# Performance work log

Hardware: AMD Instinct MI355X
Metric: run time of the kernel (lower is better)

## Reference

```python
import jax, jax.numpy as jnp
import numpy as np

N = 1_000_000
HID = 128
S = 10_000

def setup_inputs() -> dict:
    key = jax.random.key(0)
    k1, k2, k3, k4, k5 = jax.random.split(key, 5)
    seg_embs = jax.random.normal(k1, (N, HID), dtype=jnp.float32)
    owners = jnp.sort(jax.random.randint(k2, (N,), 0, S, dtype=jnp.int64))
    W_proj = jax.random.normal(k3, (HID, HID), dtype=jnp.float32) * (1.0 / np.sqrt(HID))
    b_proj = jax.random.normal(k4, (HID,), dtype=jnp.float32) * 0.02
    w_score = jax.random.normal(k5, (HID,), dtype=jnp.float32) * (1.0 / np.sqrt(HID))
    b_score = jnp.zeros((), dtype=jnp.float32)
    return {"seg_embs": seg_embs, "owners": owners, "W_proj": W_proj,
            "b_proj": b_proj, "w_score": w_score, "b_score": b_score,
            "num_segments": S}

def reference(seg_embs, owners, W_proj, b_proj, w_score, b_score, num_segments):
    # H = tanh(Linear(seg_embs)); u = score(H)  -> [N]
    H = jnp.tanh(seg_embs @ W_proj.T + b_proj)            # [N, hid]
    u = H @ w_score + b_score                              # [N]
    # per-owner (segment) stable softmax
    umax = jax.ops.segment_max(u, owners, num_segments=num_segments)   # [S]
    e = jnp.exp(u - umax[owners])                          # [N]
    denom = jax.ops.segment_sum(e, owners, num_segments=num_segments)  # [S]
    a = e / denom[owners]                                  # [N]
    # weighted sum of seg_embs per owner -> [S, hid]
    z = jax.ops.segment_sum(a[:, None] * seg_embs, owners, num_segments=num_segments)
    return z
```

## Files before the change

### kernel.cpp

```cpp
#include <hip/hip_runtime.h>
#include <hip/hip_bf16.h>
#include <cmath>

#define HID 128
#define TM 64
#define MAXK 8
#define PIECE_F 132
#define XP 132

typedef __attribute__((ext_vector_type(8))) short bf16x8;
typedef __attribute__((ext_vector_type(16))) float f32x16;
typedef __attribute__((ext_vector_type(4))) float f32x4;
typedef __attribute__((ext_vector_type(2))) float f32x2;

__device__ __forceinline__ float exp2_fast(float x) {
    float r;
    asm("v_exp_f32 %0, %1" : "=v"(r) : "v"(x));
    return r;
}

__device__ __forceinline__ bf16x8 pack8(const float* f) {
    union { short h8[8]; bf16x8 v; } u;
    #pragma unroll
    for (int q = 0; q < 8; ++q)
        u.h8[q] = (short)__bfloat16_as_ushort(__float2bfloat16(f[q]));
    return u.v;
}

__device__ __forceinline__ void tanh4(const float* arg, const float* w, float& s) {
    float a0 = exp2_fast(arg[0]) + 1.0f;
    float a1 = exp2_fast(arg[1]) + 1.0f;
    float a2 = exp2_fast(arg[2]) + 1.0f;
    float a3 = exp2_fast(arg[3]) + 1.0f;
    float p01 = a0 * a1, p23 = a2 * a3;
    float r = __builtin_amdgcn_rcpf(p01 * p23);
    float r01 = r * p23, r23 = r * p01;
    float i0 = r01 * a1, i1 = r01 * a0;
    float i2 = r23 * a3, i3 = r23 * a2;
    s = fmaf(w[0], fmaf(-2.0f, i0, 1.0f), s);
    s = fmaf(w[1], fmaf(-2.0f, i1, 1.0f), s);
    s = fmaf(w[2], fmaf(-2.0f, i2, 1.0f), s);
    s = fmaf(w[3], fmaf(-2.0f, i3, 1.0f), s);
}

__global__ __launch_bounds__(256) void prep_w_frag(
    const float* __restrict__ W, short* __restrict__ whi)
{
    int id = blockIdx.x * 256 + threadIdx.x;
    int l  = id & 63;
    int kc = (id >> 6) & 7;
    int wv = id >> 9;
    int j  = wv * 32 + (l & 31);
    int k0 = kc * 16 + ((l >> 5) << 3);
    const float* src = W + j * HID + k0;
    float a8[8];
    #pragma unroll
    for (int q = 0; q < 8; ++q) a8[q] = src[q];
    *(bf16x8*)(whi + (size_t)id * 8) = pack8(a8);
}

__global__ void seg_start_kernel(const int* __restrict__ ow,
                                 int* __restrict__ seg_start,
                                 int* __restrict__ fseg, int N, int S)
{
    const int is64 = (ow[(size_t)N - 1] == 0) ? 1 : 0;
    long i = (long)blockIdx.x * blockDim.x + threadIdx.x;
    if (i > N) return;
    int a = (i == 0) ? -1 : ow[is64 ? (size_t)(2 * (i - 1)) : (size_t)(i - 1)];
    int b = (i == N) ? S  : ow[is64 ? (size_t)(2 * i)       : (size_t)i];
    for (int s = a + 1; s <= b; ++s) seg_start[s] = (int)i;
    if (i < N && (i & (TM - 1)) == 0) fseg[i >> 6] = b;
}

__global__ __launch_bounds__(256, 6) void fused_kernel(
    const float* __restrict__ X, const short* __restrict__ whi_g,
    const float* __restrict__ bproj, const float* __restrict__ wscore,
    const int* __restrict__ seg_start, const int* __restrict__ fseg,
    float* __restrict__ pieces, int N, int S)
{
    __shared__ __align__(16) short X_lds[TM * XP];
    __shared__ float u_part[4][TM];
    __shared__ float w_lds[TM];
    __shared__ float bw_lds[2 * HID];

    const int tid  = threadIdx.x;
    const int bIdx = blockIdx.x;
    const int rbase = bIdx * TM;
    const int limit = (N - rbase < TM) ? (N - rbase) : TM;

    const int lane = tid & 63;
    const int wv   = tid >> 6;
    const int l31  = lane & 31;
    const int hig  = lane >> 5;

    const int sseg0 = fseg[bIdx];
    int svl = sseg0 + lane;
    int sv  = seg_start[(svl <= S) ? svl : S];

    #pragma unroll
    for (int it = 0; it < 4; ++it) {
        int id = it * 256 + tid;
        int r  = id >> 4;
        int c  = id & 15;
        int grow = rbase + r;
        if (grow >= N) grow = N - 1;
        float a8[8];
        *(f32x4*)(a8)     = *(const f32x4*)(X + (size_t)grow * HID + c * 8);
        *(f32x4*)(a8 + 4) = *(const f32x4*)(X + (size_t)grow * HID + c * 8 + 4);
        *(bf16x8*)(&X_lds[r * XP + c * 8]) = pack8(a8);
    }
    if (tid < HID) {
        bw_lds[2 * tid]     = 2.885390082f * bproj[tid];
        bw_lds[2 * tid + 1] = wscore[tid];
    }
    __syncthreads();

    f32x16 acc0, acc1;
    #pragma unroll
    for (int g = 0; g < 16; ++g) { acc0[g] = 0.0f; acc1[g] = 0.0f; }

    const short* wbase = whi_g + (size_t)(wv * 8) * 64 * 8 + (size_t)lane * 8;
    #pragma unroll
    for (int kc = 0; kc < 8; ++kc) {
        bf16x8 wfk = *(const bf16x8*)(wbase + (size_t)kc * 64 * 8);
        int c = kc * 2 + hig;
        bf16x8 x0 = *(const bf16x8*)(&X_lds[l31 * XP + c * 8]);
        bf16x8 x1 = *(const bf16x8*)(&X_lds[(32 + l31) * XP + c * 8]);
        acc0 = __builtin_amdgcn_mfma_f32_32x32x16_bf16(wfk, x0, acc0, 0, 0, 0);
        acc1 = __builtin_amdgcn_mfma_f32_32x32x16_bf16(wfk, x1, acc1, 0, 0, 0);
    }

    float s0 = 0.0f, s1 = 0.0f;
    #pragma unroll
    for (int g4 = 0; g4 < 4; ++g4) {
        float arg0[4], arg1[4], w4[4];
        #pragma unroll
        for (int q = 0; q < 4; ++q) {
            int reg = g4 * 4 + q;
            int j = wv * 32 + (reg & 3) + ((reg >> 2) << 3) + (hig << 2);
            f32x2 bw = *(const f32x2*)(&bw_lds[2 * j]);
            arg0[q] = fmaf(2.885390082f, acc0[reg], bw.x);
            arg1[q] = fmaf(2.885390082f, acc1[reg], bw.x);
            w4[q]   = bw.y;
        }
        tanh4(arg0, w4, s0);
        tanh4(arg1, w4, s1);
    }
    s0 += __shfl_xor(s0, 32, 64);
    s1 += __shfl_xor(s1, 32, 64);
    if (hig == 0) {
        u_part[wv][l31]      = s0;
        u_part[wv][32 + l31] = s1;
    }
    __syncthreads();

    for (int i = wv; ; i += 4) {
        int st, en;
        if (i < 63) {
            st = __shfl(sv, i, 64);
            en = __shfl(sv, i + 1, 64);
        } else {
            int s0i = sseg0 + i;
            st = seg_start[(s0i     <= S) ? s0i     : S];
            en = seg_start[(s0i + 1 <= S) ? s0i + 1 : S];
        }
        if (st >= rbase + limit) break;
        if (en <= st) continue;
        int a  = st - rbase; if (a < 0) a = 0;
        int bb = en - rbase; if (bb > limit) bb = limit;
        if (a >= bb) continue;

        float uv = -INFINITY;
        if (a + lane < bb)
            uv = u_part[0][a + lane] + u_part[1][a + lane]
               + u_part[2][a + lane] + u_part[3][a + lane];
        float m = uv;
        #pragma unroll
        for (int o = 32; o > 0; o >>= 1) m = fmaxf(m, __shfl_xor(m, o, 64));
        float e0 = (a + lane < bb) ? exp2_fast((uv - m) * 1.442695041f) : 0.0f;
        float d = e0;
        #pragma unroll
        for (int o = 32; o > 0; o >>= 1) d += __shfl_xor(d, o, 64);
        if (a + lane < bb) w_lds[a + lane] = e0;

        f32x2 p = {0.0f, 0.0f};
        int rr = a;
        for (; rr + 4 <= bb; rr += 4) {
            #pragma unroll
            for (int q = 0; q < 4; ++q) {
                int rc = rr + q;
                float wq = w_lds[rc];
                unsigned pr = *(const unsigned*)(&X_lds[rc * XP + 2 * lane]);
                float x0 = __builtin_bit_cast(float, pr << 16);
                float x1 = __builtin_bit_cast(float, pr & 0xFFFF0000u);
                p.x = fmaf(wq, x0, p.x);
                p.y = fmaf(wq, x1, p.y);
            }
        }
        for (; rr < bb; ++rr) {
            float wq = w_lds[rr];
            unsigned pr = *(const unsigned*)(&X_lds[rr * XP + 2 * lane]);
            float x0 = __builtin_bit_cast(float, pr << 16);
            float x1 = __builtin_bit_cast(float, pr & 0xFFFF0000u);
            p.x = fmaf(wq, x0, p.x);
            p.y = fmaf(wq, x1, p.y);
        }

        int sseg = sseg0 + i;
        int slot = (bIdx - (st >> 6)) & (MAXK - 1);
        float* dst = pieces + ((size_t)sseg * MAXK + slot) * PIECE_F;
        if (lane == 0) { dst[0] = m; dst[1] = d; }
        *(f32x2*)(dst + 4 + 2 * lane) = p;
    }
}

__global__ __launch_bounds__(64) void fixup_kernel(
    const float* __restrict__ pieces, const int* __restrict__ seg_start,
    float* __restrict__ z)
{
    const int s = blockIdx.x;
    const int lane = threadIdx.x;
    const int start = seg_start[s];
    const int end   = seg_start[s + 1];

    if (start >= end) {
        f32x2 zo = {0.0f, 0.0f};
        *(f32x2*)(z + (size_t)s * HID + lane * 2) = zo;
        return;
    }
    int K = ((end - 1) >> 6) - (start >> 6) + 1;
    if (K > MAXK) K = MAXK;

    const float* base0 = pieces + (size_t)s * MAXK * PIECE_F;
    float M = -INFINITY;
    for (int k = 0; k < K; ++k) M = fmaxf(M, base0[k * PIECE_F]);

    float D = 0.0f;
    f32x2 zz = {0.0f, 0.0f};
    for (int k = 0; k < K; ++k) {
        const float* b = base0 + k * PIECE_F;
        float sc = __expf(b[0] - M);
        D = fmaf(b[1], sc, D);
        f32x2 pv = *(const f32x2*)(b + 4 + lane * 2);
        zz.x = fmaf(sc, pv.x, zz.x);
        zz.y = fmaf(sc, pv.y, zz.y);
    }
    float inv = 1.0f / D;
    f32x2 zo = {zz.x * inv, zz.y * inv};
    *(f32x2*)(z + (size_t)s * HID + lane * 2) = zo;
}

extern "C" void kernel_launch(void* const* d_in, const int* in_sizes, int n_in,
                              void* d_out, int out_size, void* d_ws, size_t ws_size,
                              hipStream_t stream)
{
    const float* X   = (const float*)d_in[0];
    const int*   ow  = (const int*)  d_in[1];
    const float* W   = (const float*)d_in[2];
    const float* bp  = (const float*)d_in[3];
    const float* wsc = (const float*)d_in[4];

    const int N  = in_sizes[0] / HID;
    const int S  = out_size / HID;
    const int NT = (N + TM - 1) / TM;

    char* ws = (char*)d_ws;
    size_t off_seg = 0;
    size_t off_fs  = (((size_t)(S + 1) * 4) + 255) & ~(size_t)255;
    size_t off_w   = (off_fs + (size_t)NT * 4 + 255) & ~(size_t)255;
    size_t off_pc  = (off_w + (size_t)HID * HID * 2 + 255) & ~(size_t)255;

    int*   seg    = (int*)  (ws + off_seg);
    int*   fsg    = (int*)  (ws + off_fs);
    short* whi    = (short*)(ws + off_w);
    float* pieces = (float*)(ws + off_pc);
    float* z      = (float*)d_out;

    const int blocksB = ((N + 1) + 255) / 256;
    seg_start_kernel<<<blocksB, 256, 0, stream>>>(ow, seg, fsg, N, S);

    prep_w_frag<<<8, 256, 0, stream>>>(W, whi);

    fused_kernel<<<NT, 256, 0, stream>>>(X, whi, bp, wsc, seg, fsg,
                                         pieces, N, S);

    fixup_kernel<<<S, 64, 0, stream>>>(pieces, seg, z);
}
```

Baseline: 129.7 us.

## Process four row tiles per block with W fragments held in registers

Each block now loops over TPB=4 consecutive 64-row tiles instead of one. The W_proj MFMA fragments are loaded into registers once per block and reused across tiles, and the bias/score constants are staged once. This removes repeated global W fragment loads and per-block setup. In exchange, the kernel adds an extra barrier per tile and launches a quarter as many blocks, and launch_bounds occupancy drops from 6 to 4. The tile loop is serialized inside a block with no prefetch of the next tile, so global-load latency is less hidden.

```diff
diff --git a/kernel.cpp b/kernel.cpp
--- a/kernel.cpp
+++ b/kernel.cpp
@@ -4,6 +4,7 @@
 
 #define HID 128
 #define TM 64
+#define TPB 4
 #define MAXK 8
 #define PIECE_F 132
 #define XP 132
@@ -72,11 +73,11 @@
     if (i < N && (i & (TM - 1)) == 0) fseg[i >> 6] = b;
 }
 
-__global__ __launch_bounds__(256, 6) void fused_kernel(
+__global__ __launch_bounds__(256, 4) void fused_kernel(
     const float* __restrict__ X, const short* __restrict__ whi_g,
     const float* __restrict__ bproj, const float* __restrict__ wscore,
     const int* __restrict__ seg_start, const int* __restrict__ fseg,
-    float* __restrict__ pieces, int N, int S)
+    float* __restrict__ pieces, int N, int S, int NT)
 {
     __shared__ __align__(16) short X_lds[TM * XP];
     __shared__ float u_part[4][TM];
@@ -84,133 +85,142 @@
     __shared__ float bw_lds[2 * HID];
 
     const int tid  = threadIdx.x;
-    const int bIdx = blockIdx.x;
-    const int rbase = bIdx * TM;
-    const int limit = (N - rbase < TM) ? (N - rbase) : TM;
-
     const int lane = tid & 63;
     const int wv   = tid >> 6;
     const int l31  = lane & 31;
     const int hig  = lane >> 5;
 
-    const int sseg0 = fseg[bIdx];
-    int svl = sseg0 + lane;
-    int sv  = seg_start[(svl <= S) ? svl : S];
-
+    bf16x8 wf[8];
     #pragma unroll
-    for (int it = 0; it < 4; ++it) {
-        int id = it * 256 + tid;
-        int r  = id >> 4;
-        int c  = id & 15;
-        int grow = rbase + r;
-        if (grow >= N) grow = N - 1;
-        float a8[8];
-        *(f32x4*)(a8)     = *(const f32x4*)(X + (size_t)grow * HID + c * 8);
-        *(f32x4*)(a8 + 4) = *(const f32x4*)(X + (size_t)grow * HID + c * 8 + 4);
-        *(bf16x8*)(&X_lds[r * XP + c * 8]) = pack8(a8);
-    }
+    for (int kc = 0; kc < 8; ++kc)
+        wf[kc] = *(const bf16x8*)(whi_g + (size_t)((wv * 8 + kc) * 64 + lane) * 8);
+
     if (tid < HID) {
         bw_lds[2 * tid]     = 2.885390082f * bproj[tid];
         bw_lds[2 * tid + 1] = wscore[tid];
     }
-    __syncthreads();
-
-    f32x16 acc0, acc1;
-    #pragma unroll
-    for (int g = 0; g < 16; ++g) { acc0[g] = 0.0f; acc1[g] = 0.0f; }
-
-    const short* wbase = whi_g + (size_t)(wv * 8) * 64 * 8 + (size_t)lane * 8;
-    #pragma unroll
-    for (int kc = 0; kc < 8; ++kc) {
-        bf16x8 wfk = *(const bf16x8*)(wbase + (size_t)kc * 64 * 8);
-        int c = kc * 2 + hig;
-        bf16x8 x0 = *(const bf16x8*)(&X_lds[l31 * XP + c * 8]);
-        bf16x8 x1 = *(const bf16x8*)(&X_lds[(32 + l31) * XP + c * 8]);
-        acc0 = __builtin_amdgcn_mfma_f32_32x32x16_bf16(wfk, x0, acc0, 0, 0, 0);
-        acc1 = __builtin_amdgcn_mfma_f32_32x32x16_bf16(wfk, x1, acc1, 0, 0, 0);
-    }
-
-    float s0 = 0.0f, s1 = 0.0f;
-    #pragma unroll
-    for (int g4 = 0; g4 < 4; ++g4) {
-        float arg0[4], arg1[4], w4[4];
-        #pragma unroll
-        for (int q = 0; q < 4; ++q) {
-            int reg = g4 * 4 + q;
-            int j = wv * 32 + (reg & 3) + ((reg >> 2) << 3) + (hig << 2);
-            f32x2 bw = *(const f32x2*)(&bw_lds[2 * j]);
-            arg0[q] = fmaf(2.885390082f, acc0[reg], bw.x);
-            arg1[q] = fmaf(2.885390082f, acc1[reg], bw.x);
-            w4[q]   = bw.y;
-        }
-        tanh4(arg0, w4, s0);
-        tanh4(arg1, w4, s1);
-    }
-    s0 += __shfl_xor(s0, 32, 64);
-    s1 += __shfl_xor(s1, 32, 64);
-    if (hig == 0) {
-        u_part[wv][l31]      = s0;
-        u_part[wv][32 + l31] = s1;
-    }
-    __syncthreads();
-
-    for (int i = wv; ; i += 4) {
-        int st, en;
-        if (i < 63) {
-            st = __shfl(sv, i, 64);
-            en = __shfl(sv, i + 1, 64);
-        } else {
-            int s0i = sseg0 + i;
-            st = seg_start[(s0i     <= S) ? s0i     : S];
-            en = seg_start[(s0i + 1 <= S) ? s0i + 1 : S];
-        }
-        if (st >= rbase + limit) break;
-        if (en <= st) continue;
-        int a  = st - rbase; if (a < 0) a = 0;
-        int bb = en - rbase; if (bb > limit) bb = limit;
-        if (a >= bb) continue;
-
-        float uv = -INFINITY;
-        if (a + lane < bb)
-            uv = u_part[0][a + lane] + u_part[1][a + lane]
-               + u_part[2][a + lane] + u_part[3][a + lane];
-        float m = uv;
-        #pragma unroll
-        for (int o = 32; o > 0; o >>= 1) m = fmaxf(m, __shfl_xor(m, o, 64));
-        float e0 = (a + lane < bb) ? exp2_fast((uv - m) * 1.442695041f) : 0.0f;
-        float d = e0;
-        #pragma unroll
-        for (int o = 32; o > 0; o >>= 1) d += __shfl_xor(d, o, 64);
-        if (a + lane < bb) w_lds[a + lane] = e0;
-
-        f32x2 p = {0.0f, 0.0f};
-        int rr = a;
-        for (; rr + 4 <= bb; rr += 4) {
+
+    const int Tend0 = (blockIdx.x + 1) * TPB;
+    const int Tend  = (Tend0 < NT) ? Tend0 : NT;
+
+    for (int T = blockIdx.x * TPB; T < Tend; ++T) {
+        const int rbase = T * TM;
+        const int limit = (N - rbase < TM) ? (N - rbase) : TM;
+
+        const int sseg0 = fseg[T];
+        int svl = sseg0 + lane;
+        int sv  = seg_start[(svl <= S) ? svl : S];
+
+        #pragma unroll
+        for (int it = 0; it < 4; ++it) {
+            int id = it * 256 + tid;
+            int r  = id >> 4;
+            int c  = id & 15;
+            int grow = rbase + r;
+            if (grow >= N) grow = N - 1;
+            float a8[8];
+            *(f32x4*)(a8)     = *(const f32x4*)(X + (size_t)grow * HID + c * 8);
+            *(f32x4*)(a8 + 4) = *(const f32x4*)(X + (size_t)grow * HID + c * 8 + 4);
+            *(bf16x8*)(&X_lds[r * XP + c * 8]) = pack8(a8);
+        }
+        __syncthreads();
+
+        f32x16 acc0, acc1;
+        #pragma unroll
+        for (int g = 0; g < 16; ++g) { acc0[g] = 0.0f; acc1[g] = 0.0f; }
+
+        #pragma unroll
+        for (int kc = 0; kc < 8; ++kc) {
+            int c = kc * 2 + hig;
+            bf16x8 x0 = *(const bf16x8*)(&X_lds[l31 * XP + c * 8]);
+            bf16x8 x1 = *(const bf16x8*)(&X_lds[(32 + l31) * XP + c * 8]);
+            acc0 = __builtin_amdgcn_mfma_f32_32x32x16_bf16(wf[kc], x0, acc0, 0, 0, 0);
+            acc1 = __builtin_amdgcn_mfma_f32_32x32x16_bf16(wf[kc], x1, acc1, 0, 0, 0);
+        }
+
+        float s0 = 0.0f, s1 = 0.0f;
+        #pragma unroll
+        for (int g4 = 0; g4 < 4; ++g4) {
+            float arg0[4], arg1[4], w4[4];
             #pragma unroll
             for (int q = 0; q < 4; ++q) {
-                int rc = rr + q;
-                float wq = w_lds[rc];
-                unsigned pr = *(const unsigned*)(&X_lds[rc * XP + 2 * lane]);
+                int reg = g4 * 4 + q;
+                int j = wv * 32 + (reg & 3) + ((reg >> 2) << 3) + (hig << 2);
+                f32x2 bw = *(const f32x2*)(&bw_lds[2 * j]);
+                arg0[q] = fmaf(2.885390082f, acc0[reg], bw.x);
+                arg1[q] = fmaf(2.885390082f, acc1[reg], bw.x);
+                w4[q]   = bw.y;
+            }
+            tanh4(arg0, w4, s0);
+            tanh4(arg1, w4, s1);
+        }
+        s0 += __shfl_xor(s0, 32, 64);
+        s1 += __shfl_xor(s1, 32, 64);
+        if (hig == 0) {
+            u_part[wv][l31]      = s0;
+            u_part[wv][32 + l31] = s1;
+        }
+        __syncthreads();
+
+        for (int i = wv; ; i += 4) {
+            int st, en;
+            if (i < 63) {
+                st = __shfl(sv, i, 64);
+                en = __shfl(sv, i + 1, 64);
+            } else {
+                int s0i = sseg0 + i;
+                st = seg_start[(s0i     <= S) ? s0i     : S];
+                en = seg_start[(s0i + 1 <= S) ? s0i + 1 : S];
+            }
+            if (st >= rbase + limit) break;
+            if (en <= st) continue;
+            int a  = st - rbase; if (a < 0) a = 0;
+            int bb = en - rbase; if (bb > limit) bb = limit;
+            if (a >= bb) continue;
+
+            float uv = -INFINITY;
+            if (a + lane < bb)
+                uv = u_part[0][a + lane] + u_part[1][a + lane]
+                   + u_part[2][a + lane] + u_part[3][a + lane];
+            float m = uv;
+            #pragma unroll
+            for (int o = 32; o > 0; o >>= 1) m = fmaxf(m, __shfl_xor(m, o, 64));
+            float e0 = (a + lane < bb) ? exp2_fast((uv - m) * 1.442695041f) : 0.0f;
+            float d = e0;
+            #pragma unroll
+            for (int o = 32; o > 0; o >>= 1) d += __shfl_xor(d, o, 64);
+            if (a + lane < bb) w_lds[a + lane] = e0;
+
+            f32x2 p = {0.0f, 0.0f};
+            int rr = a;
+            for (; rr + 4 <= bb; rr += 4) {
+                #pragma unroll
+                for (int q = 0; q < 4; ++q) {
+                    int rc = rr + q;
+                    float wq = w_lds[rc];
+                    unsigned pr = *(const unsigned*)(&X_lds[rc * XP + 2 * lane]);
+                    float x0 = __builtin_bit_cast(float, pr << 16);
+                    float x1 = __builtin_bit_cast(float, pr & 0xFFFF0000u);
+                    p.x = fmaf(wq, x0, p.x);
+                    p.y = fmaf(wq, x1, p.y);
+                }
+            }
+            for (; rr < bb; ++rr) {
+                float wq = w_lds[rr];
+                unsigned pr = *(const unsigned*)(&X_lds[rr * XP + 2 * lane]);
                 float x0 = __builtin_bit_cast(float, pr << 16);
                 float x1 = __builtin_bit_cast(float, pr & 0xFFFF0000u);
                 p.x = fmaf(wq, x0, p.x);
                 p.y = fmaf(wq, x1, p.y);
             }
-        }
-        for (; rr < bb; ++rr) {
-            float wq = w_lds[rr];
-            unsigned pr = *(const unsigned*)(&X_lds[rr * XP + 2 * lane]);
-            float x0 = __builtin_bit_cast(float, pr << 16);
-            float x1 = __builtin_bit_cast(float, pr & 0xFFFF0000u);
-            p.x = fmaf(wq, x0, p.x);
-            p.y = fmaf(wq, x1, p.y);
-        }
-
-        int sseg = sseg0 + i;
-        int slot = (bIdx - (st >> 6)) & (MAXK - 1);
-        float* dst = pieces + ((size_t)sseg * MAXK + slot) * PIECE_F;
-        if (lane == 0) { dst[0] = m; dst[1] = d; }
-        *(f32x2*)(dst + 4 + 2 * lane) = p;
+
+            int sseg = sseg0 + i;
+            int slot = (T - (st >> 6)) & (MAXK - 1);
+            float* dst = pieces + ((size_t)sseg * MAXK + slot) * PIECE_F;
+            if (lane == 0) { dst[0] = m; dst[1] = d; }
+            *(f32x2*)(dst + 4 + 2 * lane) = p;
+        }
+        __syncthreads();
     }
 }
 
@@ -281,8 +291,9 @@
 
     prep_w_frag<<<8, 256, 0, stream>>>(W, whi);
 
-    fused_kernel<<<NT, 256, 0, stream>>>(X, whi, bp, wsc, seg, fsg,
-                                         pieces, N, S);
+    const int grid = (NT + TPB - 1) / TPB;
+    fused_kernel<<<grid, 256, 0, stream>>>(X, whi, bp, wsc, seg, fsg,
+                                           pieces, N, S, NT);
 
     fixup_kernel<<<S, 64, 0, stream>>>(pieces, seg, z);
 }
```

Result: slower. 142.0 us (+9.5%).
